# Kernel tuning notes

Measured on AMD Instinct MI355X. Metric: run time of the kernel, lower is better.

## Reference

```python
import jax, jax.numpy as jnp
import numpy as np

WINDOW = (16, 16)
STRIDE = (8, 8)
PADDING = (0, 0)  # (pad_h, pad_w), applied symmetrically like torch _pair semantics


def setup_inputs() -> dict:
    key = jax.random.key(0)
    x = jax.random.normal(key, (16, 3, 512, 512), dtype=jnp.float32)
    return {"x": x}


def reference(x) -> jnp.ndarray:
    wh, ww = WINDOW
    sh, sw = STRIDE
    ph, pw = PADDING
    if ph or pw:
        x = jnp.pad(x, ((0, 0), (0, 0), (ph, ph), (pw, pw)))
    B, C, H, W = x.shape
    nH = (H - wh) // sh + 1
    nW = (W - ww) // sw + 1
    # overlapping window gather indices
    rows = (jnp.arange(nH) * sh)[:, None] + jnp.arange(wh)[None, :]  # (nH, wh)
    cols = (jnp.arange(nW) * sw)[:, None] + jnp.arange(ww)[None, :]  # (nW, ww)
    # gather: (B, C, nH, nW, wh, ww)
    p = x[:, :, rows[:, None, :, None], cols[None, :, None, :]]
    # permute to (B, nH, nW, C, wh, ww) then flatten patch grid -> (B, N, C, wh, ww)
    p = jnp.transpose(p, (0, 2, 3, 1, 4, 5))
    return p.reshape(B, nH * nW, C, wh, ww)
```

## Files before the change

kernel.cpp:

```cpp
#include <hip/hip_runtime.h>


#define BB 16
#define CC 3
#define HH 512
#define WW 512
#define NH 63
#define NW 63
#define NP (NH * NW)
#define TOTAL4 (BB * NP * CC * 16 * 4)

__global__ __launch_bounds__(256) void extract_patches_kernel(
    const float* __restrict__ x, float* __restrict__ out) {
  unsigned int idx = blockIdx.x * 256u + threadIdx.x;
  if (idx >= (unsigned int)TOTAL4) return;

  unsigned int j4 = idx & 3u;
  unsigned int t  = idx >> 2;
  unsigned int i  = t & 15u;
  t >>= 4;
  unsigned int c  = t % CC;
  t /= CC;
  unsigned int p  = t % NP;
  unsigned int b  = t / NP;
  unsigned int ph = p / NW;
  unsigned int pw = p % NW;

  unsigned int row = ph * 8u + i;
  unsigned int col = pw * 8u + j4 * 4u;

  const float4* src = reinterpret_cast<const float4*>(
      x + (((size_t)(b * CC + c) * HH + row) * WW + col));
  reinterpret_cast<float4*>(out)[idx] = *src;
}

extern "C" void kernel_launch(void* const* d_in, const int* in_sizes, int n_in,
                              void* d_out, int out_size, void* d_ws, size_t ws_size,
                              hipStream_t stream) {
  const float* x = (const float*)d_in[0];
  float* out = (float*)d_out;
  dim3 grid((TOTAL4 + 255) / 256);
  extract_patches_kernel<<<grid, 256, 0, stream>>>(x, out);
}
```

Measured before the change: 241.6 us.

## Stage 16-row input strips in LDS and emit patches with nontemporal stores

Each block loads one 16-row strip of a channel into shared memory once, then writes all 63 overlapping patches of that patch-row from LDS. This removes the repeated global reads of overlapping windows and most of the per-element div/mod index math. Output uses nontemporal stores to avoid cache pollution. It adds a block barrier, and the grid is smaller (3024 blocks) with fixed LDS per block.

```diff
diff --git a/kernel.cpp b/kernel.cpp
--- a/kernel.cpp
+++ b/kernel.cpp
@@ -8,30 +8,45 @@
 #define NH 63
 #define NW 63
 #define NP (NH * NW)
-#define TOTAL4 (BB * NP * CC * 16 * 4)
+#define WIN 16
+#define STR 8
+#define LDSW 520
 
-__global__ __launch_bounds__(256) void extract_patches_kernel(
+typedef float f4 __attribute__((ext_vector_type(4)));
+
+__global__ __launch_bounds__(256) void extract_patches_lds(
     const float* __restrict__ x, float* __restrict__ out) {
-  unsigned int idx = blockIdx.x * 256u + threadIdx.x;
-  if (idx >= (unsigned int)TOTAL4) return;
+  __shared__ float lds[WIN * LDSW];
 
-  unsigned int j4 = idx & 3u;
-  unsigned int t  = idx >> 2;
-  unsigned int i  = t & 15u;
-  t >>= 4;
-  unsigned int c  = t % CC;
-  t /= CC;
-  unsigned int p  = t % NP;
-  unsigned int b  = t / NP;
-  unsigned int ph = p / NW;
-  unsigned int pw = p % NW;
+  unsigned int blk = blockIdx.x;
+  unsigned int ph = blk % NH;
+  unsigned int t2 = blk / NH;
+  unsigned int c  = t2 % CC;
+  unsigned int b  = t2 / CC;
+  unsigned int tid = threadIdx.x;
 
-  unsigned int row = ph * 8u + i;
-  unsigned int col = pw * 8u + j4 * 4u;
+  const f4* src = reinterpret_cast<const f4*>(
+      x + (((size_t)(b * CC + c) * HH + ph * STR) * WW));
+  #pragma unroll
+  for (int k = 0; k < 8; ++k) {
+    unsigned int idx  = tid + k * 256u;
+    f4 v = src[idx];
+    unsigned int row  = idx >> 7;
+    unsigned int col4 = idx & 127u;
+    *reinterpret_cast<f4*>(&lds[row * LDSW + col4 * 4u]) = v;
+  }
+  __syncthreads();
 
-  const float4* src = reinterpret_cast<const float4*>(
-      x + (((size_t)(b * CC + c) * HH + row) * WW + col));
-  reinterpret_cast<float4*>(out)[idx] = *src;
+  f4* dst = reinterpret_cast<f4*>(out) +
+            (((size_t)b * NP + (size_t)ph * NW) * CC + c) * 64u;
+  for (unsigned int u = tid; u < NW * 64u; u += 256u) {
+    unsigned int pw = u >> 6;
+    unsigned int r  = u & 63u;
+    unsigned int i  = r >> 2;
+    unsigned int j4 = r & 3u;
+    f4 v = *reinterpret_cast<const f4*>(&lds[i * LDSW + pw * STR + j4 * 4u]);
+    __builtin_nontemporal_store(v, &dst[(size_t)pw * (CC * 64u) + r]);
+  }
 }
 
 extern "C" void kernel_launch(void* const* d_in, const int* in_sizes, int n_in,
@@ -39,6 +54,6 @@
                               hipStream_t stream) {
   const float* x = (const float*)d_in[0];
   float* out = (float*)d_out;
-  dim3 grid((TOTAL4 + 255) / 256);
-  extract_patches_kernel<<<grid, 256, 0, stream>>>(x, out);
+  dim3 grid(BB * CC * NH);
+  extract_patches_lds<<<grid, 256, 0, stream>>>(x, out);
 }
```

After: 226.1 us. -6.4%, faster.
